# Kernel tuning notes

Measured on AMD Instinct MI355X. Metric: run time of the kernel, lower is better.

Reference implementation:

```python
import jax, jax.numpy as jnp
import numpy as np

B, E, S, H = 4, 1024, 2048, 16  # batch, dim, seq_len, n_heads


def setup_inputs() -> dict:
    key = jax.random.key(0)
    ks = jax.random.split(key, 7)
    x = jax.random.normal(ks[0], (B, E, S), dtype=jnp.float32)
    in_w = jax.random.normal(ks[1], (E, E), dtype=jnp.float32) * (1.0 / np.sqrt(E))
    in_b = jnp.zeros((E,), dtype=jnp.float32)
    out_w = jax.random.normal(ks[2], (E, E), dtype=jnp.float32) * (1.0 / np.sqrt(E))
    out_b = jnp.zeros((E,), dtype=jnp.float32)
    mix_w = jax.random.normal(ks[3], (H, S), dtype=jnp.float32)
    mix_b = jnp.zeros((H, S), dtype=jnp.float32)
    return {"x": x, "in_w": in_w, "in_b": in_b, "out_w": out_w,
            "out_b": out_b, "mix_w": mix_w, "mix_b": mix_b}


def _head_matrices(mix_w):
    # First H/2 heads: column-repeat causal M[i,j] = v[j] if j >= i else 0.
    # Last  H/2 heads: row-repeat causal    M[i,j] = v[i] if j >= i else 0.
    idx = jnp.arange(S)
    mask = idx[None, :] >= idx[:, None]  # (S, S), True where j >= i
    Wcol = jnp.where(mask[None], mix_w[: H // 2, None, :], jnp.zeros((), mix_w.dtype))
    Wrow = jnp.where(mask[None], mix_w[H // 2 :, :, None], jnp.zeros((), mix_w.dtype))
    return jnp.concatenate([Wcol, Wrow], axis=0)  # (H, S, S)


def reference(x, in_w, in_b, out_w, out_b, mix_w, mix_b):
    e = E // H  # per-head channel dim
    xt = jnp.transpose(x, (0, 2, 1))           # b t e
    xt = xt @ in_w.T + in_b                    # in_proj
    # 'b t (h e) -> b h e t'
    p = jnp.transpose(xt.reshape(B, S, H, e), (0, 2, 3, 1))
    Wm = _head_matrices(mix_w)                 # (H, S, S)
    # bmm per (batch, head): (e, S) @ (S, S)
    out = jnp.einsum('bhet,hts->bhes', p, Wm) + mix_b[None, :, None, :]
    # 'b h e t -> b t (h e)'
    out = jnp.transpose(out, (0, 3, 1, 2)).reshape(B, S, E)
    out = out @ out_w.T + out_b                # out_proj
    return jnp.transpose(out, (0, 2, 1))       # b e t
```

## Files before the change

kernel.cpp:

```cpp
#include <hip/hip_runtime.h>

#define B_ 4
#define E_ 1024
#define S_ 2048
#define H_ 16
#define K_ 1024

#define NCH 32
#define CS  (S_/NCH)

typedef __bf16 bf16x8 __attribute__((ext_vector_type(8)));
typedef float  f32x4  __attribute__((ext_vector_type(4)));

#define AS1 __attribute__((address_space(1)))
#define AS3 __attribute__((address_space(3)))

__device__ __forceinline__ unsigned short f2bf(float f) {
  unsigned u = __float_as_uint(f);
  u += 0x7fffu + ((u >> 16) & 1u);
  return (unsigned short)(u >> 16);
}
__device__ __forceinline__ float bf2f(unsigned short h) {
  return __uint_as_float(((unsigned)h) << 16);
}

__global__ __launch_bounds__(256)
void tc_kernel(const float* __restrict__ x, unsigned short* __restrict__ xt,
               const float* __restrict__ inw, const float* __restrict__ outw,
               unsigned short* __restrict__ w1, unsigned short* __restrict__ w2)
{
  if (blockIdx.z == 4) {
    const int per = (E_ * E_) / 4;
    const int fid = blockIdx.y * 32 + blockIdx.x;
#pragma unroll
    for (int k = 0; k < 4; ++k) {
      int i = fid * 1024 + k * 256 + threadIdx.x;
      const float4* src = (i < per) ? (const float4*)inw : (const float4*)outw;
      unsigned short* dst = (i < per) ? w1 : w2;
      int j = (i < per) ? i : i - per;
      float4 v = src[j];
      ushort4 o;
      o.x = f2bf(v.x); o.y = f2bf(v.y); o.z = f2bf(v.z); o.w = f2bf(v.w);
      *(ushort4*)(dst + (long)j * 4) = o;
    }
    return;
  }

  __shared__ float t[64][65];
  const int b  = blockIdx.z;
  const int e0 = blockIdx.y * 64;
  const int s0 = blockIdx.x * 64;
  const int tx = threadIdx.x & 63, ty = threadIdx.x >> 6;

  const float* xp = x + ((long)b * E_ + e0) * S_ + s0;
#pragma unroll
  for (int r = 0; r < 16; ++r) {
    int row = r * 4 + ty;
    t[row][tx] = xp[(long)row * S_ + tx];
  }
  __syncthreads();
  unsigned short* xo = xt + ((long)b * S_ + s0) * E_ + e0;
#pragma unroll
  for (int p = 0; p < 2; ++p) {
    int s = p * 32 + (threadIdx.x >> 3);
    int e = (threadIdx.x & 7) * 8;
    unsigned short v[8];
#pragma unroll
    for (int j = 0; j < 8; ++j) v[j] = f2bf(t[e + j][s]);
    *(ushort4*)(xo + (long)s * E_ + e)     = make_ushort4(v[0], v[1], v[2], v[3]);
    *(ushort4*)(xo + (long)s * E_ + e + 4) = make_ushort4(v[4], v[5], v[6], v[7]);
  }
}

__device__ __forceinline__ void stage_half(char* lds, const unsigned short* __restrict__ base,
                                           int kt, int ks, int tid) {
  int row = tid >> 2;
  int cb  = (tid & 3) << 4;
  int cbs = cb ^ (((row >> 1) & 3) << 4);
  const unsigned short* src = base + (long)row * K_ + kt + ks * 32 + (cbs >> 1);
  __builtin_amdgcn_global_load_lds((const AS1 void*)src,
      (AS3 void*)(lds + ks * 8192 + tid * 16), 16, 0, 0);
}

__device__ __forceinline__ void stage_tile(char* buf, const unsigned short* __restrict__ Ab,
                                           const unsigned short* __restrict__ Bb,
                                           int kt, int tid) {
  stage_half(buf,         Ab, kt, 0, tid);
  stage_half(buf,         Ab, kt, 1, tid);
  stage_half(buf + 16384, Bb, kt, 0, tid);
  stage_half(buf + 16384, Bb, kt, 1, tid);
}

template<int VARIANT>
__global__ __launch_bounds__(512, 4)
void gemm_hw(const unsigned short* __restrict__ A, const unsigned short* __restrict__ Bw,
             void* __restrict__ Cout, const float* __restrict__ bias,
             const float* __restrict__ mixw, float* __restrict__ part)
{
  __shared__ char smem[65536];

  const int tid  = threadIdx.x;
  const int lane = tid & 63, wid = tid >> 6;
  const int wm = wid >> 2, wn = wid & 3;
  const int lr = lane & 15, lg = lane >> 4;

  const int bid = blockIdx.x;
  const int xcd = bid & 7;
  const int j   = bid >> 3;
  const int tm  = (xcd << 3) | (j & 7);
  const int tn  = j >> 3;

  const unsigned short* Ab = A  + (long)tm * 128 * K_;
  const unsigned short* Bb = Bw + (long)tn * 128 * K_;

  f32x4 acc[4][2] = {};

  stage_tile(smem, Ab, Bb, 0, tid);
  __syncthreads();

  for (int t = 0; t < 16; ++t) {
    char* cur = smem + (t & 1) * 32768;
    char* nxt = smem + ((t + 1) & 1) * 32768;
    if (t + 1 < 16) stage_tile(nxt, Ab, Bb, (t + 1) * 64, tid);

#pragma unroll
    for (int ks = 0; ks < 2; ++ks) {
      bf16x8 af[4], bfv[2];
#pragma unroll
      for (int mf = 0; mf < 4; ++mf) {
        int row = wm * 64 + mf * 16 + lr;
        int cb  = (lg * 16) ^ (((row >> 1) & 3) << 4);
        af[mf] = *(const bf16x8*)(cur + ks * 8192 + row * 64 + cb);
      }
#pragma unroll
      for (int nf = 0; nf < 2; ++nf) {
        int row = wn * 32 + nf * 16 + lr;
        int cb  = (lg * 16) ^ (((row >> 1) & 3) << 4);
        bfv[nf] = *(const bf16x8*)(cur + 16384 + ks * 8192 + row * 64 + cb);
      }
#pragma unroll
      for (int mf = 0; mf < 4; ++mf)
#pragma unroll
        for (int nf = 0; nf < 2; ++nf)
          acc[mf][nf] = __builtin_amdgcn_mfma_f32_16x16x32_bf16(
              af[mf], bfv[nf], acc[mf][nf], 0, 0, 0);
    }
    __syncthreads();
  }

  if constexpr (VARIANT == 0) {
    const int bt = tm >> 4;
    const int sb = ((tm & 15) << 7) + wm * 64;
    const int ch = ((tm & 15) << 1) + wm;
#pragma unroll
    for (int nf = 0; nf < 2; ++nf) {
      const int c = tn * 128 + wn * 32 + nf * 16 + lr;
      const float bv = bias[c];
      const int h = c >> 6;
      float sm = 0.f;
#pragma unroll
      for (int mf = 0; mf < 4; ++mf) {
#pragma unroll
        for (int jj = 0; jj < 4; ++jj) {
          const int sl = sb + mf * 16 + lg * 4 + jj;
          float v = acc[mf][nf][jj] + bv;
          ((unsigned short*)Cout)[((long)bt * S_ + sl) * E_ + c] = f2bf(v);
          sm += (h < 8) ? v : v * mixw[h * S_ + sl];
        }
      }
      sm += __shfl_xor(sm, 16, 64);
      sm += __shfl_xor(sm, 32, 64);
      if (lg == 0) part[((long)bt * NCH + ch) * E_ + c] = sm;
    }
  } else {
#pragma unroll
    for (int nf = 0; nf < 2; ++nf) {
      const int c = tn * 128 + wn * 32 + nf * 16 + lr;
      const float bv = bias[c];
#pragma unroll
      for (int mf = 0; mf < 4; ++mf) {
        const int r0 = tm * 128 + wm * 64 + mf * 16 + lg * 4;
        const int s = r0 & (S_ - 1);
        const int b = r0 >> 11;
        float4 v;
        v.x = acc[mf][nf][0] + bv; v.y = acc[mf][nf][1] + bv;
        v.z = acc[mf][nf][2] + bv; v.w = acc[mf][nf][3] + bv;
        *(float4*)((float*)Cout + ((long)b * E_ + c) * S_ + s) = v;
      }
    }
  }
}

__global__ __launch_bounds__(256)
void scan_final(const unsigned short* __restrict__ yt, const float* __restrict__ mixw,
                const float* __restrict__ mixb, const float* __restrict__ part,
                unsigned short* __restrict__ zt)
{
  const int bid = blockIdx.x;
  const int xcd = bid & 7;
  const int b   = xcd >> 1;
  const int j   = bid >> 3;
  const int ch  = ((xcd & 1) << 4) | (j & 15);
  const int c   = (j >> 4) * 256 + threadIdx.x;
  const int h   = c >> 6;

  float acc = 0.f;
  for (int p = 0; p < ch; ++p) acc += part[((long)b * NCH + p) * E_ + c];
  const unsigned short* yp = yt + ((long)b * S_ + ch * CS) * E_ + c;
  unsigned short*       zp = zt + ((long)b * S_ + ch * CS) * E_ + c;
  const float* mw = mixw + (long)h * S_ + ch * CS;
  const float* mb = mixb + (long)h * S_ + ch * CS;
  if (h < 8) {
    for (int s = 0; s < CS; ++s) {
      acc += bf2f(yp[(long)s * E_]);
      zp[(long)s * E_] = f2bf(fmaf(acc, mw[s], mb[s]));
    }
  } else {
    for (int s = 0; s < CS; ++s) {
      acc += bf2f(yp[(long)s * E_]) * mw[s];
      zp[(long)s * E_] = f2bf(acc + mb[s]);
    }
  }
}

extern "C" void kernel_launch(void* const* d_in, const int* in_sizes, int n_in,
                              void* d_out, int out_size, void* d_ws, size_t ws_size,
                              hipStream_t stream)
{
  (void)in_sizes; (void)n_in; (void)out_size; (void)ws_size;
  const float* x     = (const float*)d_in[0];
  const float* in_w  = (const float*)d_in[1];
  const float* in_b  = (const float*)d_in[2];
  const float* out_w = (const float*)d_in[3];
  const float* out_b = (const float*)d_in[4];
  const float* mix_w = (const float*)d_in[5];
  const float* mix_b = (const float*)d_in[6];

  char* ws = (char*)d_ws;
  unsigned short* Xt  = (unsigned short*)(ws);
  unsigned short* Yt  = (unsigned short*)(ws + (size_t)16 * 1024 * 1024);
  unsigned short* W1b = (unsigned short*)(ws + (size_t)32 * 1024 * 1024);
  unsigned short* W2b = (unsigned short*)(ws + (size_t)34 * 1024 * 1024);
  float*          part = (float*)(ws + (size_t)36 * 1024 * 1024);
  unsigned short* Zt  = Xt;

  tc_kernel<<<dim3(S_ / 64, E_ / 64, 5), 256, 0, stream>>>(x, Xt, in_w, out_w, W1b, W2b);

  gemm_hw<0><<<dim3(512), 512, 0, stream>>>(Xt, W1b, Yt, in_b, mix_w, part);

  scan_final<<<dim3(512), 256, 0, stream>>>(Yt, mix_w, mix_b, part, Zt);

  gemm_hw<1><<<dim3(512), 512, 0, stream>>>(Zt, W2b, d_out, out_b, nullptr, nullptr);
}
```

Measured before the change: 76.01 us.

## Rewrite GEMMs with 256x256 tiles and a fine-grained 8-phase pipelined LDS schedule

Both projection GEMMs move from 128x128 tiles with simple double buffering to 256x256 tiles, 128KB of dynamic LDS and an 8-phase schedule. Each phase interleaves half-tile global-to-LDS loads with MFMA work, using explicit vmcnt waits, barriers and s_setprio. The larger tiles raise arithmetic intensity and cut redundant global loads, and the finer schedule aims to hide load latency. The cost is only 128 blocks on a 256-CU part, so half the CUs may sit idle, plus higher register pressure and a hand-tuned wait schedule that is easy to get subtly wrong.

```diff
diff --git a/kernel.cpp b/kernel.cpp
--- a/kernel.cpp
+++ b/kernel.cpp
@@ -14,6 +14,7 @@
 
 #define AS1 __attribute__((address_space(1)))
 #define AS3 __attribute__((address_space(3)))
+#define SWZ(row) ((((row) >> 1) & 3) << 4)
 
 __device__ __forceinline__ unsigned short f2bf(float f) {
   unsigned u = __float_as_uint(f);
@@ -72,114 +73,143 @@
   }
 }
 
-__device__ __forceinline__ void stage_half(char* lds, const unsigned short* __restrict__ base,
-                                           int kt, int ks, int tid) {
-  int row = tid >> 2;
-  int cb  = (tid & 3) << 4;
-  int cbs = cb ^ (((row >> 1) & 3) << 4);
-  const unsigned short* src = base + (long)row * K_ + kt + ks * 32 + (cbs >> 1);
-  __builtin_amdgcn_global_load_lds((const AS1 void*)src,
-      (AS3 void*)(lds + ks * 8192 + tid * 16), 16, 0, 0);
-}
-
-__device__ __forceinline__ void stage_tile(char* buf, const unsigned short* __restrict__ Ab,
-                                           const unsigned short* __restrict__ Bb,
-                                           int kt, int tid) {
-  stage_half(buf,         Ab, kt, 0, tid);
-  stage_half(buf,         Ab, kt, 1, tid);
-  stage_half(buf + 16384, Bb, kt, 0, tid);
-  stage_half(buf + 16384, Bb, kt, 1, tid);
-}
+#define FENCE asm volatile("" ::: "memory")
+#define BAR do { FENCE; __builtin_amdgcn_s_barrier(); FENCE; } while (0)
+#define VM(n) asm volatile("s_waitcnt vmcnt(" #n ")" ::: "memory")
+#define NOWAIT (void)0
+#define NOST   (void)0
+
+__device__ __forceinline__ void stage_u(char* smem, int bufoff, int isB,
+                                        const unsigned short* __restrict__ base,
+                                        int t, int ks, int tid) {
+#pragma unroll
+  for (int j = 0; j < 2; ++j) {
+    int chunk = j * 512 + tid;
+    int row = chunk >> 2;
+    int cb  = (chunk & 3) << 4;
+    int cbs = cb ^ SWZ(row);
+    const unsigned short* src = base + (long)row * K_ + t * 64 + ks * 32 + (cbs >> 1);
+    __builtin_amdgcn_global_load_lds((const AS1 void*)src,
+        (AS3 void*)(smem + bufoff + isB * 32768 + ks * 16384 + chunk * 16), 16, 0, 0);
+  }
+}
+
+#define PH(BUFOFF, KS, MH, READB, STAGE, WAIT) do {                          \
+    bf16x8 af[4];                                                            \
+    _Pragma("unroll")                                                        \
+    for (int q = 0; q < 4; ++q) {                                            \
+      int row = wm * 128 + ((MH) * 4 + q) * 16 + lr;                         \
+      af[q] = *(const bf16x8*)(smem + (BUFOFF) + (KS) * 16384 + row * 64 +   \
+                               ((lg * 16) ^ SWZ(row)));                      \
+    }                                                                        \
+    if (READB) {                                                             \
+      _Pragma("unroll")                                                      \
+      for (int nf = 0; nf < 4; ++nf) {                                       \
+        int row = wn * 64 + nf * 16 + lr;                                    \
+        bfv[nf] = *(const bf16x8*)(smem + (BUFOFF) + 32768 + (KS) * 16384 +  \
+                                   row * 64 + ((lg * 16) ^ SWZ(row)));       \
+      }                                                                      \
+    }                                                                        \
+    STAGE;                                                                   \
+    WAIT;                                                                    \
+    BAR;                                                                     \
+    __builtin_amdgcn_s_setprio(1);                                           \
+    _Pragma("unroll")                                                        \
+    for (int q = 0; q < 4; ++q)                                              \
+      _Pragma("unroll")                                                      \
+      for (int nf = 0; nf < 4; ++nf)                                         \
+        acc[(MH) * 4 + q][nf] = __builtin_amdgcn_mfma_f32_16x16x32_bf16(     \
+            af[q], bfv[nf], acc[(MH) * 4 + q][nf], 0, 0, 0);                 \
+    __builtin_amdgcn_s_setprio(0);                                           \
+    BAR;                                                                     \
+  } while (0)
 
 template<int VARIANT>
-__global__ __launch_bounds__(512, 4)
-void gemm_hw(const unsigned short* __restrict__ A, const unsigned short* __restrict__ Bw,
-             void* __restrict__ Cout, const float* __restrict__ bias,
-             const float* __restrict__ mixw, float* __restrict__ part)
-{
-  __shared__ char smem[65536];
-
+__global__ __launch_bounds__(512, 2)
+void gemm8(const unsigned short* __restrict__ A, const unsigned short* __restrict__ Bw,
+           void* __restrict__ Cout, const float* __restrict__ bias,
+           const float* __restrict__ mixw, float* __restrict__ part)
+{
+  extern __shared__ char smem[];
   const int tid  = threadIdx.x;
   const int lane = tid & 63, wid = tid >> 6;
   const int wm = wid >> 2, wn = wid & 3;
   const int lr = lane & 15, lg = lane >> 4;
 
   const int bid = blockIdx.x;
-  const int xcd = bid & 7;
-  const int j   = bid >> 3;
-  const int tm  = (xcd << 3) | (j & 7);
-  const int tn  = j >> 3;
-
-  const unsigned short* Ab = A  + (long)tm * 128 * K_;
-  const unsigned short* Bb = Bw + (long)tn * 128 * K_;
-
-  f32x4 acc[4][2] = {};
-
-  stage_tile(smem, Ab, Bb, 0, tid);
-  __syncthreads();
-
-  for (int t = 0; t < 16; ++t) {
-    char* cur = smem + (t & 1) * 32768;
-    char* nxt = smem + ((t + 1) & 1) * 32768;
-    if (t + 1 < 16) stage_tile(nxt, Ab, Bb, (t + 1) * 64, tid);
-
-#pragma unroll
-    for (int ks = 0; ks < 2; ++ks) {
-      bf16x8 af[4], bfv[2];
-#pragma unroll
-      for (int mf = 0; mf < 4; ++mf) {
-        int row = wm * 64 + mf * 16 + lr;
-        int cb  = (lg * 16) ^ (((row >> 1) & 3) << 4);
-        af[mf] = *(const bf16x8*)(cur + ks * 8192 + row * 64 + cb);
-      }
-#pragma unroll
-      for (int nf = 0; nf < 2; ++nf) {
-        int row = wn * 32 + nf * 16 + lr;
-        int cb  = (lg * 16) ^ (((row >> 1) & 3) << 4);
-        bfv[nf] = *(const bf16x8*)(cur + 16384 + ks * 8192 + row * 64 + cb);
-      }
-#pragma unroll
-      for (int mf = 0; mf < 4; ++mf)
-#pragma unroll
-        for (int nf = 0; nf < 2; ++nf)
-          acc[mf][nf] = __builtin_amdgcn_mfma_f32_16x16x32_bf16(
-              af[mf], bfv[nf], acc[mf][nf], 0, 0, 0);
-    }
-    __syncthreads();
-  }
+  const int xcd = bid & 7, j = bid >> 3;
+  const int tm  = (xcd << 2) | (j & 3);
+  const int tn  = j >> 2;
+
+  const unsigned short* Ab = A  + (long)tm * 256 * K_;
+  const unsigned short* Bb = Bw + (long)tn * 256 * K_;
+
+  f32x4 acc[8][4] = {};
+  bf16x8 bfv[4];
+
+  stage_u(smem, 0,     0, Ab, 0, 0, tid);  stage_u(smem, 0,     1, Bb, 0, 0, tid);
+  stage_u(smem, 0,     0, Ab, 0, 1, tid);  stage_u(smem, 0,     1, Bb, 0, 1, tid);
+  stage_u(smem, 65536, 0, Ab, 1, 0, tid);  stage_u(smem, 65536, 1, Bb, 1, 0, tid);
+  VM(8);
+  BAR;
+
+  for (int i = 0; i < 7; ++i) {
+    const int t1 = 2 * i + 1, t2 = 2 * i + 2, t3 = 2 * i + 3;
+    PH(0,     0, 0, 1, stage_u(smem, 65536, 0, Ab, t1, 1, tid), NOWAIT);
+    PH(0,     0, 1, 0, stage_u(smem, 65536, 1, Bb, t1, 1, tid), VM(8));
+    PH(0,     1, 0, 1, stage_u(smem, 0,     0, Ab, t2, 0, tid), NOWAIT);
+    PH(0,     1, 1, 0, stage_u(smem, 0,     1, Bb, t2, 0, tid), VM(8));
+    PH(65536, 0, 0, 1, stage_u(smem, 0,     0, Ab, t2, 1, tid), NOWAIT);
+    PH(65536, 0, 1, 0, stage_u(smem, 0,     1, Bb, t2, 1, tid), VM(8));
+    PH(65536, 1, 0, 1, stage_u(smem, 65536, 0, Ab, t3, 0, tid), NOWAIT);
+    PH(65536, 1, 1, 0, stage_u(smem, 65536, 1, Bb, t3, 0, tid), VM(8));
+  }
+  PH(0,     0, 0, 1, stage_u(smem, 65536, 0, Ab, 15, 1, tid), NOWAIT);
+  PH(0,     0, 1, 0, stage_u(smem, 65536, 1, Bb, 15, 1, tid), VM(8));
+  PH(0,     1, 0, 1, NOST, NOWAIT);
+  PH(0,     1, 1, 0, NOST, VM(4));
+  PH(65536, 0, 0, 1, NOST, NOWAIT);
+  PH(65536, 0, 1, 0, NOST, VM(0));
+  PH(65536, 1, 0, 1, NOST, NOWAIT);
+  PH(65536, 1, 1, 0, NOST, NOWAIT);
 
   if constexpr (VARIANT == 0) {
-    const int bt = tm >> 4;
-    const int sb = ((tm & 15) << 7) + wm * 64;
-    const int ch = ((tm & 15) << 1) + wm;
-#pragma unroll
-    for (int nf = 0; nf < 2; ++nf) {
-      const int c = tn * 128 + wn * 32 + nf * 16 + lr;
+    const int bt  = tm >> 3;
+    const int sl0 = (tm & 7) << 8;
+    const int sb  = sl0 + wm * 128;
+    const int ch0 = ((tm & 7) << 2) + wm * 2;
+#pragma unroll
+    for (int nf = 0; nf < 4; ++nf) {
+      const int c = tn * 256 + wn * 64 + nf * 16 + lr;
       const float bv = bias[c];
       const int h = c >> 6;
-      float sm = 0.f;
-#pragma unroll
-      for (int mf = 0; mf < 4; ++mf) {
+      float sm0 = 0.f, sm1 = 0.f;
+#pragma unroll
+      for (int mf = 0; mf < 8; ++mf) {
 #pragma unroll
         for (int jj = 0; jj < 4; ++jj) {
           const int sl = sb + mf * 16 + lg * 4 + jj;
           float v = acc[mf][nf][jj] + bv;
           ((unsigned short*)Cout)[((long)bt * S_ + sl) * E_ + c] = f2bf(v);
-          sm += (h < 8) ? v : v * mixw[h * S_ + sl];
+          float w = (h < 8) ? v : v * mixw[h * S_ + sl];
+          if (mf < 4) sm0 += w; else sm1 += w;
         }
       }
-      sm += __shfl_xor(sm, 16, 64);
-      sm += __shfl_xor(sm, 32, 64);
-      if (lg == 0) part[((long)bt * NCH + ch) * E_ + c] = sm;
+      sm0 += __shfl_xor(sm0, 16, 64);  sm0 += __shfl_xor(sm0, 32, 64);
+      sm1 += __shfl_xor(sm1, 16, 64);  sm1 += __shfl_xor(sm1, 32, 64);
+      if (lg == 0) {
+        part[((long)bt * NCH + ch0)     * E_ + c] = sm0;
+        part[((long)bt * NCH + ch0 + 1) * E_ + c] = sm1;
+      }
     }
   } else {
 #pragma unroll
-    for (int nf = 0; nf < 2; ++nf) {
-      const int c = tn * 128 + wn * 32 + nf * 16 + lr;
+    for (int nf = 0; nf < 4; ++nf) {
+      const int c = tn * 256 + wn * 64 + nf * 16 + lr;
       const float bv = bias[c];
 #pragma unroll
-      for (int mf = 0; mf < 4; ++mf) {
-        const int r0 = tm * 128 + wm * 64 + mf * 16 + lg * 4;
+      for (int mf = 0; mf < 8; ++mf) {
+        const int r0 = tm * 256 + wm * 128 + mf * 16 + lg * 4;
         const int s = r0 & (S_ - 1);
         const int b = r0 >> 11;
         float4 v;
@@ -244,11 +274,14 @@
   float*          part = (float*)(ws + (size_t)36 * 1024 * 1024);
   unsigned short* Zt  = Xt;
 
+  hipFuncSetAttribute((const void*)gemm8<0>, hipFuncAttributeMaxDynamicSharedMemorySize, 131072);
+  hipFuncSetAttribute((const void*)gemm8<1>, hipFuncAttributeMaxDynamicSharedMemorySize, 131072);
+
   tc_kernel<<<dim3(S_ / 64, E_ / 64, 5), 256, 0, stream>>>(x, Xt, in_w, out_w, W1b, W2b);
 
-  gemm_hw<0><<<dim3(512), 512, 0, stream>>>(Xt, W1b, Yt, in_b, mix_w, part);
+  gemm8<0><<<dim3(128), 512, 131072, stream>>>(Xt, W1b, Yt, in_b, mix_w, part);
 
   scan_final<<<dim3(512), 256, 0, stream>>>(Yt, mix_w, mix_b, part, Zt);
 
-  gemm_hw<1><<<dim3(512), 512, 0, stream>>>(Zt, W2b, d_out, out_b, nullptr, nullptr);
-}
+  gemm8<1><<<dim3(128), 512, 131072, stream>>>(Zt, W2b, d_out, out_b, nullptr, nullptr);
+}
```

Result: slower. 110.5 us (+45.3%).
